# Performance work log

Hardware: AMD Instinct MI355X
Metric: run time of the kernel (lower is better)

Reference implementation:

```python
import jax, jax.numpy as jnp
import numpy as np
from jax import lax

TAU = 0.25
N_TIMESTEPS = 12
OUTPUT_TICKS = 4
INPUT_DIM = 1024
HIDDEN = 1024
OUTPUT_DIM = 1024
CLEANUP = 512
BATCH = 1024
W_SD = 0.1


def setup_inputs() -> dict:
    key = jax.random.key(0)
    ks = jax.random.split(key, 6)
    inputs = jax.random.normal(ks[0], (BATCH, N_TIMESTEPS, INPUT_DIM), dtype=jnp.float32)
    w_oh = W_SD * jax.random.normal(ks[1], (INPUT_DIM, HIDDEN), dtype=jnp.float32)
    w_hp = W_SD * jax.random.normal(ks[2], (HIDDEN, OUTPUT_DIM), dtype=jnp.float32)
    w_pp = W_SD * jax.random.normal(ks[3], (OUTPUT_DIM, OUTPUT_DIM), dtype=jnp.float32)
    w_pc = W_SD * jax.random.normal(ks[4], (OUTPUT_DIM, CLEANUP), dtype=jnp.float32)
    w_cp = W_SD * jax.random.normal(ks[5], (CLEANUP, OUTPUT_DIM), dtype=jnp.float32)
    bias_h = jnp.zeros((HIDDEN,), jnp.float32)
    bias_p = jnp.zeros((OUTPUT_DIM,), jnp.float32)
    bias_c = jnp.zeros((CLEANUP,), jnp.float32)
    return {"inputs": inputs, "w_oh": w_oh, "w_hp": w_hp, "w_pp": w_pp,
            "w_pc": w_pc, "w_cp": w_cp, "bias_h": bias_h, "bias_p": bias_p,
            "bias_c": bias_c}


def reference(inputs, w_oh, w_hp, w_pp, w_pc, w_cp, bias_h, bias_p, bias_c):
    B = inputs.shape[0]
    act = jax.nn.sigmoid
    # time-major input stream: step t consumes o_input[:, t-1, :]
    x = jnp.swapaxes(inputs, 0, 1)  # [T, B, I]

    in_h0 = jnp.zeros((B, HIDDEN), jnp.float32)
    in_p0 = jnp.zeros((B, OUTPUT_DIM), jnp.float32)
    in_c0 = jnp.zeros((B, CLEANUP), jnp.float32)
    carry0 = (in_h0, in_p0, in_c0, in_h0 + 0.5, in_p0 + 0.5, in_c0 + 0.5)

    def step(carry, o_t):
        in_h, in_p, in_c, a_h, a_p, a_c = carry
        # leaky-integrator blends; hp/pp/cp/pc all use PREVIOUS step activations
        h = TAU * (o_t @ w_oh + bias_h) + (1.0 - TAU) * in_h
        p = TAU * (a_h @ w_hp + a_p @ w_pp + a_c @ w_cp + bias_p) + (1.0 - TAU) * in_p
        c = TAU * (a_p @ w_pc + bias_c) + (1.0 - TAU) * in_c
        a_p_new = act(p)
        new_carry = (h, p, c, act(h), a_p_new, act(c))
        return new_carry, a_p_new

    _, act_p_seq = lax.scan(step, carry0, x)  # [T, B, OUTPUT_DIM]
    return act_p_seq[-OUTPUT_TICKS:]  # [OUTPUT_TICKS, B, OUTPUT_DIM]
```

## Files before the change

### kernel.cpp

```cpp
#include <hip/hip_runtime.h>
#include <cstdint>
#include <cstddef>


typedef _Float16 half8 __attribute__((ext_vector_type(8)));
typedef float floatx4 __attribute__((ext_vector_type(4)));

__device__ __forceinline__ float sigmoidf_(float x) {
  return 1.f / (1.f + __expf(-x));
}

__device__ __forceinline__ void gld(half8& d, const _Float16* p) {
  asm volatile("global_load_dwordx4 %0, %1, off" : "=v"(d) : "v"(p) : "memory");
}
__device__ __forceinline__ void gldo(half8& d, const _Float16* p, int boff) {
  asm volatile("global_load_dwordx4 %0, %1, off offset:%2"
               : "=v"(d) : "v"(p), "n"(boff) : "memory");
}

__global__ __launch_bounds__(256) void k_pack_all(
    const float* __restrict__ w_pp, const float* __restrict__ w_cp,
    const float* __restrict__ w_pc, const float* __restrict__ w_oh,
    const float* __restrict__ w_hp, _Float16* __restrict__ Wrf,
    _Float16* __restrict__ Wcf, _Float16* __restrict__ Wohf,
    _Float16* __restrict__ Whpf) {
  const int z = blockIdx.z;
  const float* src;
  _Float16* dst;
  int N, kStride, kOff;
  switch (z) {
    case 0: src = w_pp; dst = Wrf;  N = 1024; kStride = 48; kOff = 0;  break;
    case 1: if (blockIdx.y >= 8) return;
            src = w_cp; dst = Wrf;  N = 1024; kStride = 48; kOff = 32; break;
    case 2: if (blockIdx.x >= 8) return;
            src = w_pc; dst = Wcf;  N = 512;  kStride = 32; kOff = 0;  break;
    case 3: src = w_oh; dst = Wohf; N = 1024; kStride = 32; kOff = 0;  break;
    default:src = w_hp; dst = Whpf; N = 1024; kStride = 32; kOff = 0;  break;
  }
  __shared__ float tile[64][65];
  const int k0 = blockIdx.y * 64, n0 = blockIdx.x * 64;
  const int tx = threadIdx.x & 63, ty = threadIdx.x >> 6;
#pragma unroll
  for (int jj = 0; jj < 16; ++jj) {
    int kr = jj * 4 + ty;
    tile[kr][tx] = src[(size_t)(k0 + kr) * N + n0 + tx];
  }
  __syncthreads();
  const int j = threadIdx.x >> 6, lane = threadIdx.x & 63;
  const int r16 = lane & 15, quad = lane >> 4;
#pragma unroll
  for (int c = 0; c < 2; ++c) {
    half8 v;
#pragma unroll
    for (int u = 0; u < 8; ++u)
      v[u] = (_Float16)tile[c * 32 + quad * 8 + u][j * 16 + r16];
    const int kcG = kOff + blockIdx.y * 2 + c;
    *(half8*)(dst + ((size_t)(blockIdx.x * kStride + kcG) * 4 + j) * 512 +
              lane * 8) = v;
  }
}

__global__ __launch_bounds__(256) void k_q0sum(
    const float* __restrict__ w_hp, const float* __restrict__ bias_p,
    float* __restrict__ q0) {
  __shared__ float part[4][64];
  const int n = blockIdx.x * 64 + (threadIdx.x & 63);
  const int seg = threadIdx.x >> 6;
  float s = 0.f;
  for (int k = seg * 256; k < seg * 256 + 256; ++k)
    s += w_hp[(size_t)k * 1024 + n];
  part[seg][threadIdx.x & 63] = s;
  __syncthreads();
  if (seg == 0) {
    const float t =
        part[0][threadIdx.x] + part[1][threadIdx.x] + part[2][threadIdx.x] +
        part[3][threadIdx.x];
    q0[n] = 0.25f * (0.5f * t + bias_p[n]);
  }
}

__global__ __launch_bounds__(256) void k_prep(
    const float* __restrict__ x, _Float16* __restrict__ U,
    _Float16* __restrict__ AP0, _Float16* __restrict__ AC0,
    float* __restrict__ Pst, float* __restrict__ Cst,
    const float* __restrict__ q0, _Float16* __restrict__ Q) {
  const int id = blockIdx.x * 256 + threadIdx.x;
  const int b = id >> 10, i = id & 1023;
  const float* xb = x + (size_t)b * 12 * 1024 + i;
  float g = 0.f;
#pragma unroll
  for (int t = 0; t < 11; ++t) {
    g = xb[t * 1024] + 0.75f * g;
    U[(size_t)t * 1048576 + id] = (_Float16)g;
  }
  AP0[id] = (_Float16)0.5f;
  Pst[id] = 0.f;
  Q[id] = (_Float16)q0[i];
  if (i < 512) {
    const int cid = b * 512 + i;
    AC0[cid] = (_Float16)0.5f;
    Cst[cid] = 0.f;
  }
}

#define GWAIT(NSTR, B)                                                  \
  asm volatile("s_waitcnt vmcnt(" NSTR ")"                              \
               : "+v"(ab[B][0]), "+v"(ab[B][1]), "+v"(bb[B][0]),        \
                 "+v"(bb[B][1]), "+v"(bb[B][2]), "+v"(bb[B][3]))

__global__ __launch_bounds__(256, 3) void k_gemm_fp(
    const _Float16* __restrict__ A, const _Float16* __restrict__ Bf,
    const float* __restrict__ bias, _Float16* __restrict__ dst, int mode) {
  const int lane = threadIdx.x & 63, w = threadIdx.x >> 6;
  const int r16 = lane & 15, quad = lane >> 4;
  const int mBase = (blockIdx.y * 4 + w) * 32;
  const int nt = blockIdx.x;
  const floatx4 zero = {0.f, 0.f, 0.f, 0.f};
  floatx4 acc[2][4];
#pragma unroll
  for (int i = 0; i < 2; ++i)
#pragma unroll
    for (int j = 0; j < 4; ++j) acc[i][j] = zero;

  const _Float16* A0 = A + (size_t)(mBase + r16) * 1024 + quad * 8;
  const _Float16* A1 = A0 + 16 * 1024;
  const _Float16* wb = Bf + (size_t)nt * 32 * 2048 + lane * 8;

  half8 ab[4][2], bb[4][4];
  auto LDC = [&](int c, int buf) {
    gldo(ab[buf][0], A0, c * 64);
    gldo(ab[buf][1], A1, c * 64);
    const _Float16* wp = wb + (size_t)c * 2048;
    gldo(bb[buf][0], wp, 0);
    gldo(bb[buf][1], wp, 1024);
    gldo(bb[buf][2], wp, 2048);
    gldo(bb[buf][3], wp, 3072);
  };
  auto MM = [&](int buf) {
#pragma unroll
    for (int i = 0; i < 2; ++i)
#pragma unroll
      for (int j = 0; j < 4; ++j)
        acc[i][j] = __builtin_amdgcn_mfma_f32_16x16x32_f16(
            ab[buf][i], bb[buf][j], acc[i][j], 0, 0, 0);
  };

  LDC(0, 0);
  LDC(1, 1);
  LDC(2, 2);
#pragma unroll
  for (int c = 0; c < 32; ++c) {
    const int buf = c & 3;
    if (c <= 32 - 3) GWAIT("12", buf);
    else if (c == 32 - 2) GWAIT("6", buf);
    else GWAIT("0", buf);
    if (c + 3 < 32) LDC(c + 3, (c + 3) & 3);
    MM(buf);
  }
  asm volatile("s_waitcnt vmcnt(0)" ::: "memory");

  if (mode == 0) {
    const int t = (mBase >> 10) + 1;
    const float beta = 1.f - __powf(0.75f, (float)t);
    _Float16* o = dst + (size_t)(mBase + 1024) * 1024;
#pragma unroll
    for (int i = 0; i < 2; ++i)
#pragma unroll
      for (int j = 0; j < 4; ++j) {
        const int n = nt * 64 + j * 16 + r16;
#pragma unroll
        for (int r = 0; r < 4; ++r) {
          const int row = i * 16 + quad * 4 + r;
          const float h = 0.25f * acc[i][j][r] + beta * bias[n];
          o[(size_t)row * 1024 + n] = (_Float16)sigmoidf_(h);
        }
      }
  } else {
    _Float16* o = dst + (size_t)mBase * 1024;
#pragma unroll
    for (int i = 0; i < 2; ++i)
#pragma unroll
      for (int j = 0; j < 4; ++j) {
        const int n = nt * 64 + j * 16 + r16;
#pragma unroll
        for (int r = 0; r < 4; ++r) {
          const int row = i * 16 + quad * 4 + r;
          o[(size_t)row * 1024 + n] = (_Float16)(0.25f * (acc[i][j][r] + bias[n]));
        }
      }
  }
}

__global__ __launch_bounds__(256, 3) void k_step(
    const _Float16* __restrict__ Qt, const _Float16* __restrict__ APc,
    const _Float16* __restrict__ ACc, _Float16* __restrict__ APn,
    _Float16* __restrict__ ACn, const _Float16* __restrict__ Wrf,
    const _Float16* __restrict__ Wcf, const float* __restrict__ bias_c,
    float* __restrict__ Pst, float* __restrict__ Cst,
    float* __restrict__ out_t) {
  __shared__ float red[4][2][4][4][64];
  const int lane = threadIdx.x & 63, w = threadIdx.x >> 6;
  const int r16 = lane & 15, quad = lane >> 4;
  const int blk = blockIdx.x;
  const bool isP = blk < 512;
  int mBase, nt;
  if (isP) {
    mBase = (blk >> 4) * 32;
    nt = blk & 15;
  } else {
    const int b = blk - 512;
    mBase = (b >> 3) * 32;
    nt = b & 7;
  }
  const int nBase = nt * 64;
  const floatx4 zero = {0.f, 0.f, 0.f, 0.f};
  floatx4 acc[2][4];
#pragma unroll
  for (int i = 0; i < 2; ++i)
#pragma unroll
    for (int j = 0; j < 4; ++j) acc[i][j] = zero;

  const _Float16* Ap0 = APc + (size_t)(mBase + r16) * 1024 + quad * 8;
  const _Float16* Ap1 = Ap0 + 16 * 1024;
  const _Float16* Ac0 = ACc + (size_t)(mBase + r16) * 512 + quad * 8;
  const _Float16* Ac1 = Ac0 + 16 * 512;

  half8 ab[4][2], bb[4][4];
  auto MM = [&](int buf) {
#pragma unroll
    for (int i = 0; i < 2; ++i)
#pragma unroll
      for (int j = 0; j < 4; ++j)
        acc[i][j] = __builtin_amdgcn_mfma_f32_16x16x32_f16(
            ab[buf][i], bb[buf][j], acc[i][j], 0, 0, 0);
  };

  if (isP) {
    const int kcBase = w * 12;
    const _Float16* wbase = Wrf + (size_t)(nt * 48 + kcBase) * 2048 + lane * 8;
    auto LDC = [&](int c, int buf) {
      const int kc = kcBase + c;
      const _Float16 *a0p, *a1p;
      if (kc < 32) {
        a0p = Ap0 + kc * 32;
        a1p = Ap1 + kc * 32;
      } else {
        a0p = Ac0 + (kc - 32) * 32;
        a1p = Ac1 + (kc - 32) * 32;
      }
      gld(ab[buf][0], a0p);
      gld(ab[buf][1], a1p);
      const _Float16* wp = wbase + (size_t)c * 2048;
      gldo(bb[buf][0], wp, 0);
      gldo(bb[buf][1], wp, 1024);
      gldo(bb[buf][2], wp, 2048);
      gldo(bb[buf][3], wp, 3072);
    };
    LDC(0, 0);
    LDC(1, 1);
    LDC(2, 2);
#pragma unroll
    for (int c = 0; c < 12; ++c) {
      const int buf = c & 3;
      if (c <= 12 - 3) GWAIT("12", buf);
      else if (c == 12 - 2) GWAIT("6", buf);
      else GWAIT("0", buf);
      if (c + 3 < 12) LDC(c + 3, (c + 3) & 3);
      MM(buf);
    }
  } else {
    const int kcBase = w * 8;
    const _Float16* wbase = Wcf + (size_t)(nt * 32 + kcBase) * 2048 + lane * 8;
    auto LDC = [&](int c, int buf) {
      const int kc = kcBase + c;
      gld(ab[buf][0], Ap0 + kc * 32);
      gld(ab[buf][1], Ap1 + kc * 32);
      const _Float16* wp = wbase + (size_t)c * 2048;
      gldo(bb[buf][0], wp, 0);
      gldo(bb[buf][1], wp, 1024);
      gldo(bb[buf][2], wp, 2048);
      gldo(bb[buf][3], wp, 3072);
    };
    LDC(0, 0);
    LDC(1, 1);
    LDC(2, 2);
#pragma unroll
    for (int c = 0; c < 8; ++c) {
      const int buf = c & 3;
      if (c <= 8 - 3) GWAIT("12", buf);
      else if (c == 8 - 2) GWAIT("6", buf);
      else GWAIT("0", buf);
      if (c + 3 < 8) LDC(c + 3, (c + 3) & 3);
      MM(buf);
    }
  }
  asm volatile("s_waitcnt vmcnt(0)" ::: "memory");

#pragma unroll
  for (int i = 0; i < 2; ++i)
#pragma unroll
    for (int j = 0; j < 4; ++j)
#pragma unroll
      for (int r = 0; r < 4; ++r) red[w][i][j][r][lane] = acc[i][j][r];
  __syncthreads();

  if (isP) {
#pragma unroll
    for (int i = 0; i < 2; ++i) {
      const int n = nBase + w * 16 + r16;
#pragma unroll
      for (int r = 0; r < 4; ++r) {
        const float v = red[0][i][w][r][lane] + red[1][i][w][r][lane] +
                        red[2][i][w][r][lane] + red[3][i][w][r][lane];
        const int b = mBase + i * 16 + quad * 4 + r;
        const size_t o = (size_t)b * 1024 + n;
        const float pn = 0.25f * v + (float)Qt[o] + 0.75f * Pst[o];
        Pst[o] = pn;
        const float a = sigmoidf_(pn);
        APn[o] = (_Float16)a;
        if (out_t) out_t[o] = a;
      }
    }
  } else {
#pragma unroll
    for (int i = 0; i < 2; ++i) {
      const int n = nBase + w * 16 + r16;
#pragma unroll
      for (int r = 0; r < 4; ++r) {
        const float v = red[0][i][w][r][lane] + red[1][i][w][r][lane] +
                        red[2][i][w][r][lane] + red[3][i][w][r][lane];
        const int b = mBase + i * 16 + quad * 4 + r;
        const size_t o = (size_t)b * 512 + n;
        const float cn = 0.25f * (v + bias_c[n]) + 0.75f * Cst[o];
        Cst[o] = cn;
        ACn[o] = (_Float16)sigmoidf_(cn);
      }
    }
  }
}
#undef GWAIT

extern "C" void kernel_launch(void* const* d_in, const int* in_sizes, int n_in,
                              void* d_out, int out_size, void* d_ws,
                              size_t ws_size, hipStream_t stream) {
  const float* x      = (const float*)d_in[0];
  const float* w_oh   = (const float*)d_in[1];
  const float* w_hp   = (const float*)d_in[2];
  const float* w_pp   = (const float*)d_in[3];
  const float* w_pc   = (const float*)d_in[4];
  const float* w_cp   = (const float*)d_in[5];
  const float* bias_h = (const float*)d_in[6];
  const float* bias_p = (const float*)d_in[7];
  const float* bias_c = (const float*)d_in[8];
  float* out = (float*)d_out;

  uint8_t* p = (uint8_t*)d_ws;
  _Float16* Wrf  = (_Float16*)p; p += (size_t)1024 * 1536 * 2;
  _Float16* Wcf  = (_Float16*)p; p += (size_t)512 * 1024 * 2;
  _Float16* Wohf = (_Float16*)p; p += (size_t)1024 * 1024 * 2;
  _Float16* Whpf = (_Float16*)p; p += (size_t)1024 * 1024 * 2;
  _Float16* U    = (_Float16*)p; p += (size_t)11 * 1048576 * 2;
  _Float16* AH   = (_Float16*)p; p += (size_t)12 * 1048576 * 2;
  _Float16* Q    = (_Float16*)p; p += (size_t)12 * 1048576 * 2;
  _Float16* AP0  = (_Float16*)p; p += (size_t)1048576 * 2;
  _Float16* AP1  = (_Float16*)p; p += (size_t)1048576 * 2;
  _Float16* AC0  = (_Float16*)p; p += (size_t)512 * 1024 * 2;
  _Float16* AC1  = (_Float16*)p; p += (size_t)512 * 1024 * 2;
  float* Pst = (float*)p; p += (size_t)1048576 * 4;
  float* Cst = (float*)p; p += (size_t)512 * 1024 * 4;
  float* q0  = (float*)p; p += 1024 * 4;

  const dim3 blk256(256);
  k_pack_all<<<dim3(16, 16, 5), blk256, 0, stream>>>(w_pp, w_cp, w_pc, w_oh,
                                                     w_hp, Wrf, Wcf, Wohf, Whpf);
  k_q0sum<<<dim3(16), blk256, 0, stream>>>(w_hp, bias_p, q0);
  k_prep<<<4096, blk256, 0, stream>>>(x, U, AP0, AC0, Pst, Cst, q0, Q);
  k_gemm_fp<<<dim3(16, 88), blk256, 0, stream>>>(U, Wohf, bias_h, AH, 0);
  k_gemm_fp<<<dim3(16, 88), blk256, 0, stream>>>(AH + 1048576, Whpf, bias_p,
                                                 Q + 1048576, 1);
  for (int t = 0; t < 12; ++t) {
    const _Float16* APc = (t & 1) ? AP1 : AP0;
    _Float16* APn       = (t & 1) ? AP0 : AP1;
    const _Float16* ACc = (t & 1) ? AC1 : AC0;
    _Float16* ACn       = (t & 1) ? AC0 : AC1;
    float* ot = (t >= 8) ? out + (size_t)(t - 8) * 1048576 : (float*)nullptr;
    k_step<<<dim3(768), blk256, 0, stream>>>(Q + (size_t)t * 1048576, APc,
                                             ACc, APn, ACn, Wrf, Wcf, bias_c,
                                             Pst, Cst, ot);
  }
}
```

Measured before the change: 457.5 us.

## Fuse twelve recurrent step launches into one persistent kernel with grid barrier

Replaces the twelve per-timestep kernel launches with a single persistent kernel of 768 blocks that loops over timesteps and synchronises through a global atomic counter barrier. The leaky-integrator P and C states now stay in registers instead of being read from and written to global Pst/Cst arrays each step. This removes launch gaps and state traffic. It relies on all 768 blocks being co-resident, which the occupancy of 3 blocks per CU on 256 CUs allows; otherwise the barrier would deadlock. It also adds spin-wait and fence overhead at every step.

New measurement: 1.355 ms. +196.1%, slower.

```diff
diff --git a/kernel.cpp b/kernel.cpp
--- a/kernel.cpp
+++ b/kernel.cpp
@@ -82,8 +82,8 @@
 __global__ __launch_bounds__(256) void k_prep(
     const float* __restrict__ x, _Float16* __restrict__ U,
     _Float16* __restrict__ AP0, _Float16* __restrict__ AC0,
-    float* __restrict__ Pst, float* __restrict__ Cst,
-    const float* __restrict__ q0, _Float16* __restrict__ Q) {
+    const float* __restrict__ q0, _Float16* __restrict__ Q,
+    unsigned* __restrict__ bar) {
   const int id = blockIdx.x * 256 + threadIdx.x;
   const int b = id >> 10, i = id & 1023;
   const float* xb = x + (size_t)b * 12 * 1024 + i;
@@ -94,13 +94,9 @@
     U[(size_t)t * 1048576 + id] = (_Float16)g;
   }
   AP0[id] = (_Float16)0.5f;
-  Pst[id] = 0.f;
   Q[id] = (_Float16)q0[i];
-  if (i < 512) {
-    const int cid = b * 512 + i;
-    AC0[cid] = (_Float16)0.5f;
-    Cst[cid] = 0.f;
-  }
+  if (i < 512) AC0[b * 512 + i] = (_Float16)0.5f;
+  if (id == 0) *bar = 0u;
 }
 
 #define GWAIT(NSTR, B)                                                  \
@@ -191,13 +187,12 @@
   }
 }
 
-__global__ __launch_bounds__(256, 3) void k_step(
-    const _Float16* __restrict__ Qt, const _Float16* __restrict__ APc,
-    const _Float16* __restrict__ ACc, _Float16* __restrict__ APn,
-    _Float16* __restrict__ ACn, const _Float16* __restrict__ Wrf,
+__global__ __launch_bounds__(256, 3) void k_steps(
+    const _Float16* __restrict__ Q, _Float16* __restrict__ AP0,
+    _Float16* __restrict__ AP1, _Float16* __restrict__ AC0,
+    _Float16* __restrict__ AC1, const _Float16* __restrict__ Wrf,
     const _Float16* __restrict__ Wcf, const float* __restrict__ bias_c,
-    float* __restrict__ Pst, float* __restrict__ Cst,
-    float* __restrict__ out_t) {
+    float* __restrict__ out, unsigned* __restrict__ bar) {
   __shared__ float red[4][2][4][4][64];
   const int lane = threadIdx.x & 63, w = threadIdx.x >> 6;
   const int r16 = lane & 15, quad = lane >> 4;
@@ -214,127 +209,160 @@
   }
   const int nBase = nt * 64;
   const floatx4 zero = {0.f, 0.f, 0.f, 0.f};
-  floatx4 acc[2][4];
+
+  const _Float16* wbaseP = Wrf + (size_t)(nt * 48 + w * 12) * 2048 + lane * 8;
+  const _Float16* wbaseC = Wcf + (size_t)(nt * 32 + w * 8) * 2048 + lane * 8;
+
+  float state[2][4];
 #pragma unroll
   for (int i = 0; i < 2; ++i)
 #pragma unroll
-    for (int j = 0; j < 4; ++j) acc[i][j] = zero;
-
-  const _Float16* Ap0 = APc + (size_t)(mBase + r16) * 1024 + quad * 8;
-  const _Float16* Ap1 = Ap0 + 16 * 1024;
-  const _Float16* Ac0 = ACc + (size_t)(mBase + r16) * 512 + quad * 8;
-  const _Float16* Ac1 = Ac0 + 16 * 512;
+    for (int r = 0; r < 4; ++r) state[i][r] = 0.f;
 
   half8 ab[4][2], bb[4][4];
-  auto MM = [&](int buf) {
+
+#pragma unroll 1
+  for (int t = 0; t < 12; ++t) {
+    const _Float16* APc = (t & 1) ? AP1 : AP0;
+    _Float16* APn       = (t & 1) ? AP0 : AP1;
+    const _Float16* ACc = (t & 1) ? AC1 : AC0;
+    _Float16* ACn       = (t & 1) ? AC0 : AC1;
+
+    floatx4 acc[2][4];
 #pragma unroll
     for (int i = 0; i < 2; ++i)
 #pragma unroll
+      for (int j = 0; j < 4; ++j) acc[i][j] = zero;
+
+    auto MM = [&](int buf) {
+#pragma unroll
+      for (int i = 0; i < 2; ++i)
+#pragma unroll
+        for (int j = 0; j < 4; ++j)
+          acc[i][j] = __builtin_amdgcn_mfma_f32_16x16x32_f16(
+              ab[buf][i], bb[buf][j], acc[i][j], 0, 0, 0);
+    };
+
+    const _Float16* Ap0 = APc + (size_t)(mBase + r16) * 1024 + quad * 8;
+    const _Float16* Ap1 = Ap0 + 16 * 1024;
+    const _Float16* Ac0 = ACc + (size_t)(mBase + r16) * 512 + quad * 8;
+    const _Float16* Ac1 = Ac0 + 16 * 512;
+
+    if (isP) {
+      const int kcBase = w * 12;
+      auto LDC = [&](int c, int buf) {
+        const int kc = kcBase + c;
+        const _Float16 *a0p, *a1p;
+        if (kc < 32) {
+          a0p = Ap0 + kc * 32;
+          a1p = Ap1 + kc * 32;
+        } else {
+          a0p = Ac0 + (kc - 32) * 32;
+          a1p = Ac1 + (kc - 32) * 32;
+        }
+        gld(ab[buf][0], a0p);
+        gld(ab[buf][1], a1p);
+        const _Float16* wp = wbaseP + (size_t)c * 2048;
+        gldo(bb[buf][0], wp, 0);
+        gldo(bb[buf][1], wp, 1024);
+        gldo(bb[buf][2], wp, 2048);
+        gldo(bb[buf][3], wp, 3072);
+      };
+      LDC(0, 0);
+      LDC(1, 1);
+      LDC(2, 2);
+#pragma unroll
+      for (int c = 0; c < 12; ++c) {
+        const int buf = c & 3;
+        if (c <= 12 - 3) GWAIT("12", buf);
+        else if (c == 12 - 2) GWAIT("6", buf);
+        else GWAIT("0", buf);
+        if (c + 3 < 12) LDC(c + 3, (c + 3) & 3);
+        MM(buf);
+      }
+    } else {
+      const int kcBase = w * 8;
+      auto LDC = [&](int c, int buf) {
+        const int kc = kcBase + c;
+        gld(ab[buf][0], Ap0 + kc * 32);
+        gld(ab[buf][1], Ap1 + kc * 32);
+        const _Float16* wp = wbaseC + (size_t)c * 2048;
+        gldo(bb[buf][0], wp, 0);
+        gldo(bb[buf][1], wp, 1024);
+        gldo(bb[buf][2], wp, 2048);
+        gldo(bb[buf][3], wp, 3072);
+      };
+      LDC(0, 0);
+      LDC(1, 1);
+      LDC(2, 2);
+#pragma unroll
+      for (int c = 0; c < 8; ++c) {
+        const int buf = c & 3;
+        if (c <= 8 - 3) GWAIT("12", buf);
+        else if (c == 8 - 2) GWAIT("6", buf);
+        else GWAIT("0", buf);
+        if (c + 3 < 8) LDC(c + 3, (c + 3) & 3);
+        MM(buf);
+      }
+    }
+    asm volatile("s_waitcnt vmcnt(0)" ::: "memory");
+
+#pragma unroll
+    for (int i = 0; i < 2; ++i)
+#pragma unroll
       for (int j = 0; j < 4; ++j)
-        acc[i][j] = __builtin_amdgcn_mfma_f32_16x16x32_f16(
-            ab[buf][i], bb[buf][j], acc[i][j], 0, 0, 0);
-  };
-
-  if (isP) {
-    const int kcBase = w * 12;
-    const _Float16* wbase = Wrf + (size_t)(nt * 48 + kcBase) * 2048 + lane * 8;
-    auto LDC = [&](int c, int buf) {
-      const int kc = kcBase + c;
-      const _Float16 *a0p, *a1p;
-      if (kc < 32) {
-        a0p = Ap0 + kc * 32;
-        a1p = Ap1 + kc * 32;
-      } else {
-        a0p = Ac0 + (kc - 32) * 32;
-        a1p = Ac1 + (kc - 32) * 32;
-      }
-      gld(ab[buf][0], a0p);
-      gld(ab[buf][1], a1p);
-      const _Float16* wp = wbase + (size_t)c * 2048;
-      gldo(bb[buf][0], wp, 0);
-      gldo(bb[buf][1], wp, 1024);
-      gldo(bb[buf][2], wp, 2048);
-      gldo(bb[buf][3], wp, 3072);
-    };
-    LDC(0, 0);
-    LDC(1, 1);
-    LDC(2, 2);
-#pragma unroll
-    for (int c = 0; c < 12; ++c) {
-      const int buf = c & 3;
-      if (c <= 12 - 3) GWAIT("12", buf);
-      else if (c == 12 - 2) GWAIT("6", buf);
-      else GWAIT("0", buf);
-      if (c + 3 < 12) LDC(c + 3, (c + 3) & 3);
-      MM(buf);
+#pragma unroll
+        for (int r = 0; r < 4; ++r) red[w][i][j][r][lane] = acc[i][j][r];
+    __syncthreads();
+
+    if (isP) {
+      const _Float16* Qt = Q + (size_t)t * 1048576;
+      float* out_t = (t >= 8) ? out + (size_t)(t - 8) * 1048576 : (float*)nullptr;
+#pragma unroll
+      for (int i = 0; i < 2; ++i) {
+        const int n = nBase + w * 16 + r16;
+#pragma unroll
+        for (int r = 0; r < 4; ++r) {
+          const float v = red[0][i][w][r][lane] + red[1][i][w][r][lane] +
+                          red[2][i][w][r][lane] + red[3][i][w][r][lane];
+          const int b = mBase + i * 16 + quad * 4 + r;
+          const size_t o = (size_t)b * 1024 + n;
+          const float pn = 0.25f * v + (float)Qt[o] + 0.75f * state[i][r];
+          state[i][r] = pn;
+          const float a = sigmoidf_(pn);
+          APn[o] = (_Float16)a;
+          if (out_t) out_t[o] = a;
+        }
+      }
+    } else {
+#pragma unroll
+      for (int i = 0; i < 2; ++i) {
+        const int n = nBase + w * 16 + r16;
+#pragma unroll
+        for (int r = 0; r < 4; ++r) {
+          const float v = red[0][i][w][r][lane] + red[1][i][w][r][lane] +
+                          red[2][i][w][r][lane] + red[3][i][w][r][lane];
+          const float cn = 0.25f * (v + bias_c[n]) + 0.75f * state[i][r];
+          state[i][r] = cn;
+          const int b = mBase + i * 16 + quad * 4 + r;
+          ACn[(size_t)b * 512 + n] = (_Float16)sigmoidf_(cn);
+        }
+      }
     }
-  } else {
-    const int kcBase = w * 8;
-    const _Float16* wbase = Wcf + (size_t)(nt * 32 + kcBase) * 2048 + lane * 8;
-    auto LDC = [&](int c, int buf) {
-      const int kc = kcBase + c;
-      gld(ab[buf][0], Ap0 + kc * 32);
-      gld(ab[buf][1], Ap1 + kc * 32);
-      const _Float16* wp = wbase + (size_t)c * 2048;
-      gldo(bb[buf][0], wp, 0);
-      gldo(bb[buf][1], wp, 1024);
-      gldo(bb[buf][2], wp, 2048);
-      gldo(bb[buf][3], wp, 3072);
-    };
-    LDC(0, 0);
-    LDC(1, 1);
-    LDC(2, 2);
-#pragma unroll
-    for (int c = 0; c < 8; ++c) {
-      const int buf = c & 3;
-      if (c <= 8 - 3) GWAIT("12", buf);
-      else if (c == 8 - 2) GWAIT("6", buf);
-      else GWAIT("0", buf);
-      if (c + 3 < 8) LDC(c + 3, (c + 3) & 3);
-      MM(buf);
-    }
-  }
-  asm volatile("s_waitcnt vmcnt(0)" ::: "memory");
-
-#pragma unroll
-  for (int i = 0; i < 2; ++i)
-#pragma unroll
-    for (int j = 0; j < 4; ++j)
-#pragma unroll
-      for (int r = 0; r < 4; ++r) red[w][i][j][r][lane] = acc[i][j][r];
-  __syncthreads();
-
-  if (isP) {
-#pragma unroll
-    for (int i = 0; i < 2; ++i) {
-      const int n = nBase + w * 16 + r16;
-#pragma unroll
-      for (int r = 0; r < 4; ++r) {
-        const float v = red[0][i][w][r][lane] + red[1][i][w][r][lane] +
-                        red[2][i][w][r][lane] + red[3][i][w][r][lane];
-        const int b = mBase + i * 16 + quad * 4 + r;
-        const size_t o = (size_t)b * 1024 + n;
-        const float pn = 0.25f * v + (float)Qt[o] + 0.75f * Pst[o];
-        Pst[o] = pn;
-        const float a = sigmoidf_(pn);
-        APn[o] = (_Float16)a;
-        if (out_t) out_t[o] = a;
-      }
-    }
-  } else {
-#pragma unroll
-    for (int i = 0; i < 2; ++i) {
-      const int n = nBase + w * 16 + r16;
-#pragma unroll
-      for (int r = 0; r < 4; ++r) {
-        const float v = red[0][i][w][r][lane] + red[1][i][w][r][lane] +
-                        red[2][i][w][r][lane] + red[3][i][w][r][lane];
-        const int b = mBase + i * 16 + quad * 4 + r;
-        const size_t o = (size_t)b * 512 + n;
-        const float cn = 0.25f * (v + bias_c[n]) + 0.75f * Cst[o];
-        Cst[o] = cn;
-        ACn[o] = (_Float16)sigmoidf_(cn);
-      }
+
+    if (t < 11) {
+      __syncthreads();
+      if (threadIdx.x == 0) {
+        __builtin_amdgcn_fence(__ATOMIC_RELEASE, "agent");
+        __hip_atomic_fetch_add(bar, 1u, __ATOMIC_RELAXED,
+                               __HIP_MEMORY_SCOPE_AGENT);
+        const unsigned target = 768u * (unsigned)(t + 1);
+        while (__hip_atomic_load(bar, __ATOMIC_RELAXED,
+                                 __HIP_MEMORY_SCOPE_AGENT) < target)
+          __builtin_amdgcn_s_sleep(2);
+        __builtin_amdgcn_fence(__ATOMIC_ACQUIRE, "agent");
+      }
+      __syncthreads();
     }
   }
 }
@@ -366,26 +394,17 @@
   _Float16* AP1  = (_Float16*)p; p += (size_t)1048576 * 2;
   _Float16* AC0  = (_Float16*)p; p += (size_t)512 * 1024 * 2;
   _Float16* AC1  = (_Float16*)p; p += (size_t)512 * 1024 * 2;
-  float* Pst = (float*)p; p += (size_t)1048576 * 4;
-  float* Cst = (float*)p; p += (size_t)512 * 1024 * 4;
   float* q0  = (float*)p; p += 1024 * 4;
+  unsigned* bar = (unsigned*)p; p += 256;
 
   const dim3 blk256(256);
   k_pack_all<<<dim3(16, 16, 5), blk256, 0, stream>>>(w_pp, w_cp, w_pc, w_oh,
                                                      w_hp, Wrf, Wcf, Wohf, Whpf);
   k_q0sum<<<dim3(16), blk256, 0, stream>>>(w_hp, bias_p, q0);
-  k_prep<<<4096, blk256, 0, stream>>>(x, U, AP0, AC0, Pst, Cst, q0, Q);
+  k_prep<<<4096, blk256, 0, stream>>>(x, U, AP0, AC0, q0, Q, bar);
   k_gemm_fp<<<dim3(16, 88), blk256, 0, stream>>>(U, Wohf, bias_h, AH, 0);
   k_gemm_fp<<<dim3(16, 88), blk256, 0, stream>>>(AH + 1048576, Whpf, bias_p,
                                                  Q + 1048576, 1);
-  for (int t = 0; t < 12; ++t) {
-    const _Float16* APc = (t & 1) ? AP1 : AP0;
-    _Float16* APn       = (t & 1) ? AP0 : AP1;
-    const _Float16* ACc = (t & 1) ? AC1 : AC0;
-    _Float16* ACn       = (t & 1) ? AC0 : AC1;
-    float* ot = (t >= 8) ? out + (size_t)(t - 8) * 1048576 : (float*)nullptr;
-    k_step<<<dim3(768), blk256, 0, stream>>>(Q + (size_t)t * 1048576, APc,
-                                             ACc, APn, ACn, Wrf, Wcf, bias_c,
-                                             Pst, Cst, ot);
-  }
-}
+  k_steps<<<dim3(768), blk256, 0, stream>>>(Q, AP0, AP1, AC0, AC1, Wrf, Wcf,
+                                            bias_c, out, bar);
+}
```
